# Performance work log

Hardware: AMD Instinct MI355X
Metric: run time of the kernel (lower is better)

Reference implementation:

```python
import math
import jax, jax.numpy as jnp
import numpy as np

B, N, D, H = 8, 512, 1024, 16
HD = D // H
K_DEFAULT, K_MAX, PROX_THR = 8, 12, 20.0


def setup_inputs() -> dict:
    key = jax.random.key(0)
    ks = jax.random.split(key, 12)
    tokens_B = jax.random.normal(ks[0], (B, N, D), dtype=jnp.float32)
    ego_distances = jax.random.uniform(ks[1], (B, N), dtype=jnp.float32)
    ego_mask = jnp.zeros((B, N), dtype=bool).at[:, 0].set(True)  # token 0 is ego
    ego_speed = jax.random.uniform(ks[2], (B,), dtype=jnp.float32)
    s = 1.0 / math.sqrt(D)
    Wq = jax.random.normal(ks[3], (D, D), jnp.float32) * s
    Wk = jax.random.normal(ks[4], (D, D), jnp.float32) * s
    Wv = jax.random.normal(ks[5], (D, D), jnp.float32) * s
    Weq = jax.random.normal(ks[6], (D, D), jnp.float32) * s
    Wo = jax.random.normal(ks[7], (D, D), jnp.float32) * (0.02 * s)
    Dm = D // 4
    W1 = jax.random.normal(ks[8], (Dm, 2), jnp.float32) * (1.0 / math.sqrt(2))
    b1 = jnp.zeros((Dm,), jnp.float32)
    W2 = jax.random.normal(ks[9], (H, Dm), jnp.float32) * (1.0 / math.sqrt(Dm))
    b2 = jnp.zeros((H,), jnp.float32)
    return dict(tokens_B=tokens_B, ego_distances=ego_distances, ego_mask=ego_mask,
                ego_speed=ego_speed, Wq=Wq, Wk=Wk, Wv=Wv, Weq=Weq, Wo=Wo,
                W1=W1, b1=b1, W2=W2, b2=b2)


def _compute_K(ego_speed, ego_distances):
    # deterministic, no-grad lookup (torch: @torch.no_grad)
    n = ego_distances.shape[1]
    close = (ego_distances < PROX_THR).astype(jnp.float32).sum(-1)
    density = close / max(n, 1)
    avg_speed = float(jnp.mean(ego_speed))
    avg_density = float(jnp.mean(density))
    K = K_DEFAULT
    if avg_speed > 15.0:
        K = min(K + 1, K_MAX)
    if avg_density > 0.5:
        K = min(K + 1, K_MAX)
    return min(K, n - 1)


def reference(tokens_B, ego_distances, ego_mask, ego_speed, Wq, Wk, Wv, Weq, Wo, W1, b1, W2, b2):
    b, n, d = tokens_B.shape
    K = _compute_K(ego_speed, ego_distances)
    if K <= 0:
        return jnp.zeros_like(tokens_B)

    # top-K nearest-to-ego neighbors per token, excluding self
    eye = jnp.eye(n, dtype=bool)
    dist_rank = jnp.where(eye[None, :, :], jnp.inf, ego_distances[:, None, :])  # (B,N,N)
    _, topk_idx = jax.lax.top_k(-dist_rank, K)  # (B,N,K) indices of smallest dists

    neighbors = jax.vmap(lambda t, idx: t[idx])(tokens_B, topk_idx)  # (B,N,K,D)

    is_ego = ego_mask.astype(tokens_B.dtype)[..., None]
    Q = (1.0 - is_ego) * (tokens_B @ Wq.T) + is_ego * (tokens_B @ Weq.T)
    Km = neighbors @ Wk.T
    Vm = neighbors @ Wv.T

    Q = Q.reshape(b, n, H, HD).transpose(0, 2, 1, 3)              # (B,H,N,hd)
    Km = Km.reshape(b, n, K, H, HD).transpose(0, 3, 1, 2, 4)      # (B,H,N,K,hd)
    Vm = Vm.reshape(b, n, K, H, HD).transpose(0, 3, 1, 2, 4)

    scores = jnp.einsum('bhnd,bhnkd->bhnk', Q, Km) / math.sqrt(HD)

    # additive pairwise distance bias MLP on (d_i_to_ego, d_j_to_ego)
    d_i = jnp.broadcast_to(ego_distances[:, :, None], (b, n, K))
    d_j = jax.vmap(lambda dd, idx: dd[idx])(ego_distances, topk_idx)
    dist_pair = jnp.stack([d_i, d_j], axis=-1)                    # (B,N,K,2)
    bias = jax.nn.relu(dist_pair @ W1.T + b1) @ W2.T + b2         # (B,N,K,H)
    scores = scores + bias.transpose(0, 3, 1, 2)                  # FIX-1: additive

    attn = jax.nn.softmax(scores, axis=-1)
    out = jnp.einsum('bhnk,bhnkd->bhnd', attn, Vm)
    out = out.transpose(0, 2, 1, 3).reshape(b, n, d)              # FIX-2 axis order
    return out @ Wo.T
```

## Files before the change

kernel.cpp:

```cpp
#include <hip/hip_runtime.h>
#include <math.h>

#define Bn 8
#define Nn 512
#define Dn 1024
#define Hn 16
#define HDn 64
#define KMAX 12
#define NSMAX 13
#define PROX 20.0f

typedef __attribute__((ext_vector_type(8))) short bf16x8;
typedef __attribute__((ext_vector_type(4))) float f32x4;

__device__ __forceinline__ unsigned short f2bf(float f) {
    unsigned int u = __float_as_uint(f);
    return (unsigned short)((u + 0x7FFFu + ((u >> 16) & 1u)) >> 16);
}
__device__ __forceinline__ float bf2f(unsigned short u) {
    return __uint_as_float(((unsigned int)u) << 16);
}

__global__ __launch_bounds__(256) void cvt_meta_kernel(const float* __restrict__ tokens,
                                                       const float* __restrict__ Wq,
                                                       const float* __restrict__ Wo,
                                                       const float* __restrict__ Wk,
                                                       const float* __restrict__ Wv,
                                                       const float* __restrict__ dist,
                                                       const float* __restrict__ speed,
                                                       unsigned short* __restrict__ tok_h,
                                                       unsigned short* __restrict__ wq_h,
                                                       unsigned short* __restrict__ wo_h,
                                                       unsigned short* __restrict__ wkv_h,
                                                       int* __restrict__ meta,
                                                       int* __restrict__ Lidx,
                                                       unsigned short* __restrict__ tok_g) {
    int blk = blockIdx.x;
    if (blk < 8192) {
        const float* src;
        unsigned short* dst;
        int local;
        if (blk < 4096) { src = tokens; dst = tok_h; local = blk; }
        else if (blk < 5120) { src = Wq; dst = wq_h; local = blk - 4096; }
        else if (blk < 6144) { src = Wo; dst = wo_h; local = blk - 5120; }
        else if (blk < 7168) { src = Wk; dst = wkv_h; local = blk - 6144; }
        else { src = Wv; dst = wkv_h + (size_t)Dn * Dn; local = blk - 7168; }
        int i = (local * 256 + threadIdx.x) * 4;
        float4 v = *(const float4*)&src[i];
        ushort4 o;
        o.x = f2bf(v.x); o.y = f2bf(v.y); o.z = f2bf(v.z); o.w = f2bf(v.w);
        *(ushort4*)&dst[i] = o;
        return;
    }
    if (threadIdx.x >= 64) return;
    int lane = threadIdx.x;
    int b = blk - 8192;

    int cnt = 0;
    for (int i = lane; i < Bn * Nn; i += 64) cnt += (dist[i] < PROX) ? 1 : 0;
    for (int off = 32; off; off >>= 1) cnt += __shfl_xor(cnt, off);

    float sp = 0.f;
    for (int i = lane; i < Bn; i += 64) sp += speed[i];
    for (int off = 32; off; off >>= 1) sp += __shfl_xor(sp, off);

    float avg_density = (float)cnt / (float)(Bn * Nn);
    float avg_speed = sp / (float)Bn;
    int K = 8;
    if (avg_speed > 15.0f) K = min(K + 1, KMAX);
    if (avg_density > 0.5f) K = min(K + 1, KMAX);
    K = min(K, Nn - 1);
    if (b == 0 && lane == 0) meta[0] = K;
    int ns = K + 1;

    int sel[NSMAX];
    float dloc[Nn / 64];
    #pragma unroll
    for (int j = 0; j < Nn / 64; ++j) dloc[j] = dist[b * Nn + lane + 64 * j];
    for (int r = 0; r < ns; ++r) {
        float mv = 1e30f;
        int mi = 0;
        #pragma unroll
        for (int j = 0; j < Nn / 64; ++j) {
            if (dloc[j] < mv) { mv = dloc[j]; mi = lane + 64 * j; }
        }
        for (int off = 32; off; off >>= 1) {
            float ov = __shfl_xor(mv, off);
            int oi = __shfl_xor(mi, off);
            if (ov < mv || (ov == mv && oi < mi)) { mv = ov; mi = oi; }
        }
        sel[r] = mi;
        if (lane == 0) Lidx[b * NSMAX + r] = mi;
        if ((mi & 63) == lane) dloc[mi >> 6] = 1e30f;
    }

    const float* srcp = &tokens[(size_t)(b * Nn + sel[0]) * Dn];
    float4 pre[4];
    #pragma unroll
    for (int q = 0; q < 4; ++q) pre[q] = *(const float4*)&srcp[(q * 64 + lane) * 4];
    for (int s = 0; s < ns; ++s) {
        float4 cur[4];
        #pragma unroll
        for (int q = 0; q < 4; ++q) cur[q] = pre[q];
        if (s + 1 < ns) {
            srcp = &tokens[(size_t)(b * Nn + sel[s + 1]) * Dn];
            #pragma unroll
            for (int q = 0; q < 4; ++q) pre[q] = *(const float4*)&srcp[(q * 64 + lane) * 4];
        }
        unsigned short* dst = &tok_g[(size_t)(b * 16 + s) * Dn];
        #pragma unroll
        for (int q = 0; q < 4; ++q) {
            ushort4 o;
            o.x = f2bf(cur[q].x); o.y = f2bf(cur[q].y); o.z = f2bf(cur[q].z); o.w = f2bf(cur[q].w);
            *(ushort4*)&dst[(q * 64 + lane) * 4] = o;
        }
    }
}

__device__ __forceinline__ void gemm_body_s(const unsigned short* A,
                                            const unsigned short* Bm,
                                            float* Cf, unsigned short* Ch,
                                            int Nd, int Kd, int sA, int sB,
                                            int bm, int bn, int mode, int hh,
                                            unsigned short* As, unsigned short* Bs) {
    int t = threadIdx.x;
    int wave = t >> 6, lane = t & 63;
    int wm = wave >> 1, wn = wave & 1;

    int srow = lane >> 2;
    int skoff = (lane & 3) * 8;
    const unsigned short* Ag  = A  + (size_t)(bm + wave * 16 + srow) * sA + skoff;
    const unsigned short* Bg  = Bm + (size_t)(bn + wave * 32 + srow) * sB + skoff;
    const unsigned short* Bg2 = Bg + (size_t)16 * sB;

    f32x4 acc[2][4] = {};
    int fm = lane & 15;
    int fk = (lane >> 4) * 8;

    auto stage = [&](int buf) {
        unsigned short* AsW  = As + buf * 2048 + (wave * 16) * 32;
        unsigned short* BsW  = Bs + buf * 4096 + (wave * 32) * 32;
        __builtin_amdgcn_global_load_lds((const __attribute__((address_space(1))) void*)Ag,
                                         (__attribute__((address_space(3))) void*)AsW, 16, 0, 0);
        __builtin_amdgcn_global_load_lds((const __attribute__((address_space(1))) void*)Bg,
                                         (__attribute__((address_space(3))) void*)BsW, 16, 0, 0);
        __builtin_amdgcn_global_load_lds((const __attribute__((address_space(1))) void*)Bg2,
                                         (__attribute__((address_space(3))) void*)(BsW + 512), 16, 0, 0);
        Ag += 32; Bg += 32; Bg2 += 32;
    };

    int nsteps = Kd >> 5;
    stage(0);
    __syncthreads();
    int cur = 0;
    for (int s = 0; s < nsteps; ++s) {
        if (s + 1 < nsteps) stage(cur ^ 1);
        const unsigned short* Ab = As + cur * 2048;
        const unsigned short* Bb = Bs + cur * 4096;
        bf16x8 af[2], bfr[4];
        #pragma unroll
        for (int mi = 0; mi < 2; ++mi)
            af[mi] = *(const bf16x8*)&Ab[(wm * 32 + mi * 16 + fm) * 32 + fk];
        #pragma unroll
        for (int ni = 0; ni < 4; ++ni)
            bfr[ni] = *(const bf16x8*)&Bb[(wn * 64 + ni * 16 + fm) * 32 + fk];
        #pragma unroll
        for (int mi = 0; mi < 2; ++mi)
            #pragma unroll
            for (int ni = 0; ni < 4; ++ni)
                acc[mi][ni] = __builtin_amdgcn_mfma_f32_16x16x32_bf16(af[mi], bfr[ni], acc[mi][ni], 0, 0, 0);
        __syncthreads();
        cur ^= 1;
    }

    int erow = (lane >> 4) * 4;
    #pragma unroll
    for (int mi = 0; mi < 2; ++mi)
        #pragma unroll
        for (int ni = 0; ni < 4; ++ni)
            #pragma unroll
            for (int r = 0; r < 4; ++r) {
                int row = bm + wm * 32 + mi * 16 + erow + r;
                int col = bn + wn * 64 + ni * 16 + fm;
                if (mode == 0) {
                    Cf[(size_t)row * Nd + col] = acc[mi][ni][r];
                } else if (mode == 1) {
                    Ch[(size_t)row * Nd + col] = f2bf(acc[mi][ni][r]);
                } else {
                    int bb = col >> 4, ss = col & 15;
                    Ch[((size_t)bb * 1024 + row) * 256 + ss * 16 + hh] = f2bf(acc[mi][ni][r]);
                }
            }
}

__global__ __launch_bounds__(256) void proj_fused_kernel(const unsigned short* __restrict__ tok_h,
                                                         const unsigned short* __restrict__ wq_h,
                                                         const unsigned short* __restrict__ tok_g,
                                                         const unsigned short* __restrict__ wkv_h,
                                                         const float* __restrict__ tokens,
                                                         const float* __restrict__ Weq,
                                                         unsigned short* __restrict__ Qbuf_h,
                                                         float* __restrict__ Kproj,
                                                         unsigned short* __restrict__ v_h,
                                                         float* __restrict__ Qego) {
    __shared__ unsigned short As[2 * 64 * 32];
    __shared__ unsigned short Bs[2 * 128 * 32];
    __shared__ float tok[Dn];

    int blk = blockIdx.x;
    if (blk < 16) {
        gemm_body_s(tok_g, wkv_h, Kproj, 0, Dn, Dn, Dn, Dn,
                    (blk >> 3) * 64, (blk & 7) * 128, 0, 0, As, Bs);
    } else if (blk < 32) {
        int idx = blk - 16;
        gemm_body_s(tok_g, wkv_h + (size_t)Dn * Dn, 0, v_h, Dn, Dn, Dn, Dn,
                    (idx >> 3) * 64, (idx & 7) * 128, 1, 0, As, Bs);
    } else if (blk < 544) {
        int idx = blk - 32;
        gemm_body_s(tok_h, wq_h, 0, Qbuf_h, Dn, Dn, Dn, Dn,
                    (idx >> 3) * 64, (idx & 7) * 128, 1, 0, As, Bs);
    } else {
        int blk2 = blk - 544;
        int b = blk2 >> 5, cg = blk2 & 31;
        for (int t = threadIdx.x; t < Dn; t += 256) tok[t] = tokens[(size_t)(b * Nn) * Dn + t];
        __syncthreads();
        int w = threadIdx.x >> 6, lane = threadIdx.x & 63;
        for (int o = 0; o < 8; ++o) {
            int col = cg * 32 + w * 8 + o;
            const float* wr = &Weq[(size_t)col * Dn];
            float sum = 0.f;
            #pragma unroll
            for (int q = 0; q < 4; ++q) {
                float4 w4 = *(const float4*)&wr[q * 256 + lane * 4];
                float4 t4 = *(const float4*)&tok[q * 256 + lane * 4];
                sum += w4.x * t4.x + w4.y * t4.y + w4.z * t4.z + w4.w * t4.w;
            }
            for (int off = 32; off; off >>= 1) sum += __shfl_xor(sum, off);
            if (lane == 0) Qego[(size_t)b * Dn + col] = sum;
        }
    }
}

__global__ __launch_bounds__(256) void vo3_gemm_kernel(const unsigned short* __restrict__ wo_h,
                                                       const unsigned short* __restrict__ v_h,
                                                       unsigned short* __restrict__ Vo3T) {
    __shared__ unsigned short As[2 * 64 * 32];
    __shared__ unsigned short Bs[2 * 128 * 32];
    int h = blockIdx.y;
    gemm_body_s(wo_h + h * HDn, v_h + h * HDn, 0, Vo3T, 0, HDn, Dn, Dn,
                blockIdx.x * 64, 0, 2, h, As, Bs);
}

#define HSTR 264
__global__ __launch_bounds__(64) void attn_kernel(const unsigned short* __restrict__ Qh,
                                                  const float* __restrict__ Qego,
                                                  const float* __restrict__ Kproj,
                                                  const float* __restrict__ dist,
                                                  const float* __restrict__ W1,
                                                  const float* __restrict__ b1,
                                                  const float* __restrict__ W2,
                                                  const float* __restrict__ b2,
                                                  const int* __restrict__ meta,
                                                  const int* __restrict__ Lidx,
                                                  unsigned short* __restrict__ Wt) {
    __shared__ float hid[KMAX * HSTR];
    __shared__ float sc[Hn * NSMAX];
    __shared__ float at[Hn * NSMAX];
    __shared__ int selslot[NSMAX];
    __shared__ int inv[16];
    __shared__ float dj[NSMAX];

    int bi = blockIdx.x;
    int b = bi >> 9;
    int i = bi & (Nn - 1);
    int K = meta[0];
    int ns = K + 1;
    int lane = threadIdx.x;
    int gq = lane >> 4, l = lane & 15;

    float d_i = dist[b * Nn + i];

    {
        int s = lane;
        int jj = (s < ns) ? Lidx[b * NSMAX + s] : -1;
        bool valid = (s < ns) && (jj != i);
        unsigned long long mask = __ballot(valid);
        int rank = __popcll(mask & ((1ull << s) - 1ull));
        bool take = valid && (rank < K);
        if (take) {
            selslot[rank] = s;
            dj[rank] = dist[b * Nn + jj];
        }
        if (s < 16) inv[s] = take ? rank : -1;
    }

    #pragma unroll
    for (int j = 0; j < 4; ++j) {
        int c = lane + 64 * j;
        float2 w01 = *(const float2*)&W1[2 * c];
        float bb = b1[c];
        for (int k = 0; k < K; ++k) {
            float h = w01.x * d_i + w01.y * dj[k] + bb;
            hid[k * HSTR + c] = h > 0.f ? h : 0.f;
        }
    }

    for (int gg = 0; gg < 4; ++gg) {
        int g = gq * 4 + gg;
        float4 qv;
        if (i == 0) {
            qv = *(const float4*)&Qego[(size_t)b * Dn + g * HDn + l * 4];
        } else {
            ushort4 qh = *(const ushort4*)&Qh[(size_t)bi * Dn + g * HDn + l * 4];
            qv.x = bf2f(qh.x); qv.y = bf2f(qh.y); qv.z = bf2f(qh.z); qv.w = bf2f(qh.w);
        }
        float4 w2v[4];
        #pragma unroll
        for (int ii = 0; ii < 4; ++ii)
            w2v[ii] = *(const float4*)&W2[g * 256 + ii * 64 + l * 4];
        float bias0 = b2[g];

        float4 kvn = *(const float4*)&Kproj[(size_t)(b * 16 + selslot[0]) * Dn + g * HDn + l * 4];
        for (int k = 0; k < K; ++k) {
            float4 kv4 = kvn;
            if (k + 1 < K)
                kvn = *(const float4*)&Kproj[(size_t)(b * 16 + selslot[k + 1]) * Dn + g * HDn + l * 4];
            float val = (qv.x * kv4.x + qv.y * kv4.y + qv.z * kv4.z + qv.w * kv4.w) * 0.125f;
            #pragma unroll
            for (int ii = 0; ii < 4; ++ii) {
                float4 h4 = *(const float4*)&hid[k * HSTR + ii * 64 + l * 4];
                val += w2v[ii].x * h4.x + w2v[ii].y * h4.y + w2v[ii].z * h4.z + w2v[ii].w * h4.w;
            }
            val += __shfl_xor(val, 1);
            val += __shfl_xor(val, 2);
            val += __shfl_xor(val, 4);
            val += __shfl_xor(val, 8);
            if (l == 0) sc[g * NSMAX + k] = val + bias0;
        }
    }

    #pragma unroll
    for (int hh = 0; hh < 4; ++hh) {
        int h = gq * 4 + hh;
        int k = l;
        float s = (k < K) ? sc[h * NSMAX + k] : -1e30f;
        float m = s;
        m = fmaxf(m, __shfl_xor(m, 1));
        m = fmaxf(m, __shfl_xor(m, 2));
        m = fmaxf(m, __shfl_xor(m, 4));
        m = fmaxf(m, __shfl_xor(m, 8));
        float e = (k < K) ? __expf(s - m) : 0.f;
        float ssum = e;
        ssum += __shfl_xor(ssum, 1);
        ssum += __shfl_xor(ssum, 2);
        ssum += __shfl_xor(ssum, 4);
        ssum += __shfl_xor(ssum, 8);
        if (k < K) at[h * NSMAX + k] = e / ssum;
    }

    {
        ushort4 o;
        unsigned short* op = (unsigned short*)&o;
        #pragma unroll
        for (int j = 0; j < 4; ++j) {
            int tt = lane * 4 + j;
            int s = tt >> 4, h = tt & 15;
            int k = (s < NSMAX) ? inv[s] : -1;
            float a = (k >= 0) ? at[h * NSMAX + k] : 0.f;
            op[j] = f2bf(a);
        }
        *(ushort4*)&Wt[(size_t)bi * 256 + lane * 4] = o;
    }
}

__global__ __launch_bounds__(256) void final_gemm_kernel(const unsigned short* __restrict__ Wt,
                                                         const unsigned short* __restrict__ Vo3T,
                                                         float* __restrict__ out) {
    __shared__ unsigned short As[2 * 64 * 32];
    __shared__ unsigned short Bs[2 * 128 * 32];
    int rbase = blockIdx.y * 64;
    int b = rbase >> 9;
    int bmloc = rbase & (Nn - 1);
    gemm_body_s(Wt + (size_t)b * Nn * 256,
                Vo3T + (size_t)b * Dn * 256,
                out + (size_t)b * Nn * Dn, 0,
                Dn, 256, 256, 256, bmloc, blockIdx.x * 128, 0, 0, As, Bs);
}

extern "C" void kernel_launch(void* const* d_in, const int* in_sizes, int n_in,
                              void* d_out, int out_size, void* d_ws, size_t ws_size,
                              hipStream_t stream) {
    (void)in_sizes; (void)n_in; (void)out_size; (void)ws_size;
    const float* tokens = (const float*)d_in[0];
    const float* dist   = (const float*)d_in[1];
    const float* speed  = (const float*)d_in[3];
    const float* Wq  = (const float*)d_in[4];
    const float* Wk  = (const float*)d_in[5];
    const float* Wv  = (const float*)d_in[6];
    const float* Weq = (const float*)d_in[7];
    const float* Wo  = (const float*)d_in[8];
    const float* W1  = (const float*)d_in[9];
    const float* b1  = (const float*)d_in[10];
    const float* W2  = (const float*)d_in[11];
    const float* b2  = (const float*)d_in[12];
    float* out = (float*)d_out;

    char* ws = (char*)d_ws;
    const size_t SZ_KP   = (size_t)128 * Dn * sizeof(float);
    const size_t SZ_VH   = (size_t)128 * Dn * sizeof(unsigned short);
    const size_t SZ_V3   = (size_t)Bn * Dn * 256 * sizeof(unsigned short);
    const size_t SZ_WT   = (size_t)Bn * Nn * 256 * sizeof(unsigned short);
    const size_t SZ_QH   = (size_t)Bn * Nn * Dn * sizeof(unsigned short);
    const size_t SZ_BIGH = (size_t)Bn * Nn * Dn * sizeof(unsigned short);
    const size_t SZ_WH   = (size_t)Dn * Dn * sizeof(unsigned short);
    const size_t SZ_TG   = (size_t)128 * Dn * sizeof(unsigned short);
    const size_t SZ_QE   = (size_t)Bn * Dn * sizeof(float);

    size_t off = 0;
    int*   meta  = (int*)(ws + off);  off += 256;
    int*   Lidx  = (int*)(ws + off);  off += 768;
    float* Kproj = (float*)(ws + off); off += SZ_KP;
    float* Qego  = (float*)(ws + off); off += SZ_QE;
    unsigned short* Qbuf_h = (unsigned short*)(ws + off); off += SZ_QH;
    unsigned short* v_h   = (unsigned short*)(ws + off); off += SZ_VH;
    unsigned short* Vo3T  = (unsigned short*)(ws + off); off += SZ_V3;
    unsigned short* Wt    = (unsigned short*)(ws + off); off += SZ_WT;
    unsigned short* tok_h = (unsigned short*)(ws + off); off += SZ_BIGH;
    unsigned short* wq_h  = (unsigned short*)(ws + off); off += SZ_WH;
    unsigned short* wo_h  = (unsigned short*)(ws + off); off += SZ_WH;
    unsigned short* wkv_h = (unsigned short*)(ws + off); off += 2 * SZ_WH;
    unsigned short* tok_g = (unsigned short*)(ws + off); off += SZ_TG;

    cvt_meta_kernel<<<8200, 256, 0, stream>>>(tokens, Wq, Wo, Wk, Wv, dist, speed,
                                              tok_h, wq_h, wo_h, wkv_h, meta, Lidx, tok_g);
    proj_fused_kernel<<<800, 256, 0, stream>>>(tok_h, wq_h, tok_g, wkv_h, tokens, Weq,
                                               Qbuf_h, Kproj, v_h, Qego);
    vo3_gemm_kernel<<<dim3(16, 16), 256, 0, stream>>>(wo_h, v_h, Vo3T);
    attn_kernel<<<Bn * Nn, 64, 0, stream>>>(Qbuf_h, Qego, Kproj, dist, W1, b1, W2, b2,
                                            meta, Lidx, Wt);
    final_gemm_kernel<<<dim3(Dn / 128, (Bn * Nn) / 64), 256, 0, stream>>>(Wt, Vo3T, out);
}
```

Before: 196.3 us.

## Widen attention block to one head per 16 lanes and recompute bias MLP in registers

The attention kernel goes from 64 to 256 threads per token, so each group of 16 lanes handles one head instead of looping over four. The distance-bias MLP hidden layer is no longer staged in a large shared-memory array. Each lane precomputes the d_i part of the first layer in registers and recomputes the ReLU hidden values per neighbor, which removes the roughly 12 KB hid buffer and its LDS traffic. Scores stay in registers, so the sc buffer goes away. The cost is duplicated hidden-layer arithmetic across the 16 heads, plus more registers per thread and two block barriers.

After: 184.2 us. 6.2% less time.

```diff
diff --git a/kernel.cpp b/kernel.cpp
--- a/kernel.cpp
+++ b/kernel.cpp
@@ -251,20 +251,17 @@
                 blockIdx.x * 64, 0, 2, h, As, Bs);
 }
 
-#define HSTR 264
-__global__ __launch_bounds__(64) void attn_kernel(const unsigned short* __restrict__ Qh,
-                                                  const float* __restrict__ Qego,
-                                                  const float* __restrict__ Kproj,
-                                                  const float* __restrict__ dist,
-                                                  const float* __restrict__ W1,
-                                                  const float* __restrict__ b1,
-                                                  const float* __restrict__ W2,
-                                                  const float* __restrict__ b2,
-                                                  const int* __restrict__ meta,
-                                                  const int* __restrict__ Lidx,
-                                                  unsigned short* __restrict__ Wt) {
-    __shared__ float hid[KMAX * HSTR];
-    __shared__ float sc[Hn * NSMAX];
+__global__ __launch_bounds__(256) void attn_kernel(const unsigned short* __restrict__ Qh,
+                                                   const float* __restrict__ Qego,
+                                                   const float* __restrict__ Kproj,
+                                                   const float* __restrict__ dist,
+                                                   const float* __restrict__ W1,
+                                                   const float* __restrict__ b1,
+                                                   const float* __restrict__ W2,
+                                                   const float* __restrict__ b2,
+                                                   const int* __restrict__ meta,
+                                                   const int* __restrict__ Lidx,
+                                                   unsigned short* __restrict__ Wt) {
     __shared__ float at[Hn * NSMAX];
     __shared__ int selslot[NSMAX];
     __shared__ int inv[16];
@@ -275,13 +272,36 @@
     int i = bi & (Nn - 1);
     int K = meta[0];
     int ns = K + 1;
-    int lane = threadIdx.x;
-    int gq = lane >> 4, l = lane & 15;
+    int t = threadIdx.x;
+    int g = t >> 4, l = t & 15;
 
     float d_i = dist[b * Nn + i];
 
-    {
-        int s = lane;
+    float4 qv;
+    if (i == 0) {
+        qv = *(const float4*)&Qego[(size_t)b * Dn + g * HDn + l * 4];
+    } else {
+        ushort4 qh = *(const ushort4*)&Qh[(size_t)bi * Dn + g * HDn + l * 4];
+        qv.x = bf2f(qh.x); qv.y = bf2f(qh.y); qv.z = bf2f(qh.z); qv.w = bf2f(qh.w);
+    }
+    float4 w2v[4];
+    #pragma unroll
+    for (int ii = 0; ii < 4; ++ii)
+        w2v[ii] = *(const float4*)&W2[g * 256 + ii * 64 + l * 4];
+
+    float basec[4][4], w1y[4][4];
+    #pragma unroll
+    for (int ii = 0; ii < 4; ++ii)
+        #pragma unroll
+        for (int j = 0; j < 4; ++j) {
+            int c = ii * 64 + l * 4 + j;
+            float2 w01 = *(const float2*)&W1[2 * c];
+            basec[ii][j] = w01.x * d_i + b1[c];
+            w1y[ii][j] = w01.y;
+        }
+
+    if (t < 64) {
+        int s = t;
         int jj = (s < ns) ? Lidx[b * NSMAX + s] : -1;
         bool valid = (s < ns) && (jj != i);
         unsigned long long mask = __ballot(valid);
@@ -293,83 +313,55 @@
         }
         if (s < 16) inv[s] = take ? rank : -1;
     }
-
-    #pragma unroll
-    for (int j = 0; j < 4; ++j) {
-        int c = lane + 64 * j;
-        float2 w01 = *(const float2*)&W1[2 * c];
-        float bb = b1[c];
-        for (int k = 0; k < K; ++k) {
-            float h = w01.x * d_i + w01.y * dj[k] + bb;
-            hid[k * HSTR + c] = h > 0.f ? h : 0.f;
-        }
-    }
-
-    for (int gg = 0; gg < 4; ++gg) {
-        int g = gq * 4 + gg;
-        float4 qv;
-        if (i == 0) {
-            qv = *(const float4*)&Qego[(size_t)b * Dn + g * HDn + l * 4];
-        } else {
-            ushort4 qh = *(const ushort4*)&Qh[(size_t)bi * Dn + g * HDn + l * 4];
-            qv.x = bf2f(qh.x); qv.y = bf2f(qh.y); qv.z = bf2f(qh.z); qv.w = bf2f(qh.w);
-        }
-        float4 w2v[4];
-        #pragma unroll
-        for (int ii = 0; ii < 4; ++ii)
-            w2v[ii] = *(const float4*)&W2[g * 256 + ii * 64 + l * 4];
+    __syncthreads();
+
+    float myscore = -1e30f;
+    {
         float bias0 = b2[g];
-
         float4 kvn = *(const float4*)&Kproj[(size_t)(b * 16 + selslot[0]) * Dn + g * HDn + l * 4];
         for (int k = 0; k < K; ++k) {
             float4 kv4 = kvn;
             if (k + 1 < K)
                 kvn = *(const float4*)&Kproj[(size_t)(b * 16 + selslot[k + 1]) * Dn + g * HDn + l * 4];
+            float djk = dj[k];
             float val = (qv.x * kv4.x + qv.y * kv4.y + qv.z * kv4.z + qv.w * kv4.w) * 0.125f;
             #pragma unroll
             for (int ii = 0; ii < 4; ++ii) {
-                float4 h4 = *(const float4*)&hid[k * HSTR + ii * 64 + l * 4];
-                val += w2v[ii].x * h4.x + w2v[ii].y * h4.y + w2v[ii].z * h4.z + w2v[ii].w * h4.w;
+                float h0 = basec[ii][0] + w1y[ii][0] * djk; h0 = h0 > 0.f ? h0 : 0.f;
+                float h1 = basec[ii][1] + w1y[ii][1] * djk; h1 = h1 > 0.f ? h1 : 0.f;
+                float h2 = basec[ii][2] + w1y[ii][2] * djk; h2 = h2 > 0.f ? h2 : 0.f;
+                float h3 = basec[ii][3] + w1y[ii][3] * djk; h3 = h3 > 0.f ? h3 : 0.f;
+                val += w2v[ii].x * h0 + w2v[ii].y * h1 + w2v[ii].z * h2 + w2v[ii].w * h3;
             }
             val += __shfl_xor(val, 1);
             val += __shfl_xor(val, 2);
             val += __shfl_xor(val, 4);
             val += __shfl_xor(val, 8);
-            if (l == 0) sc[g * NSMAX + k] = val + bias0;
-        }
-    }
-
-    #pragma unroll
-    for (int hh = 0; hh < 4; ++hh) {
-        int h = gq * 4 + hh;
-        int k = l;
-        float s = (k < K) ? sc[h * NSMAX + k] : -1e30f;
-        float m = s;
+            if (l == k) myscore = val + bias0;
+        }
+    }
+
+    {
+        float m = myscore;
         m = fmaxf(m, __shfl_xor(m, 1));
         m = fmaxf(m, __shfl_xor(m, 2));
         m = fmaxf(m, __shfl_xor(m, 4));
         m = fmaxf(m, __shfl_xor(m, 8));
-        float e = (k < K) ? __expf(s - m) : 0.f;
+        float e = (l < K) ? __expf(myscore - m) : 0.f;
         float ssum = e;
         ssum += __shfl_xor(ssum, 1);
         ssum += __shfl_xor(ssum, 2);
         ssum += __shfl_xor(ssum, 4);
         ssum += __shfl_xor(ssum, 8);
-        if (k < K) at[h * NSMAX + k] = e / ssum;
-    }
+        if (l < K) at[g * NSMAX + l] = e / ssum;
+    }
+    __syncthreads();
 
     {
-        ushort4 o;
-        unsigned short* op = (unsigned short*)&o;
-        #pragma unroll
-        for (int j = 0; j < 4; ++j) {
-            int tt = lane * 4 + j;
-            int s = tt >> 4, h = tt & 15;
-            int k = (s < NSMAX) ? inv[s] : -1;
-            float a = (k >= 0) ? at[h * NSMAX + k] : 0.f;
-            op[j] = f2bf(a);
-        }
-        *(ushort4*)&Wt[(size_t)bi * 256 + lane * 4] = o;
+        int s = t >> 4, h = t & 15;
+        int k = (s < NSMAX) ? inv[s] : -1;
+        float a = (k >= 0) ? at[h * NSMAX + k] : 0.f;
+        Wt[(size_t)bi * 256 + t] = f2bf(a);
     }
 }
 
@@ -436,7 +428,7 @@
     proj_fused_kernel<<<800, 256, 0, stream>>>(tok_h, wq_h, tok_g, wkv_h, tokens, Weq,
                                                Qbuf_h, Kproj, v_h, Qego);
     vo3_gemm_kernel<<<dim3(16, 16), 256, 0, stream>>>(wo_h, v_h, Vo3T);
-    attn_kernel<<<Bn * Nn, 64, 0, stream>>>(Qbuf_h, Qego, Kproj, dist, W1, b1, W2, b2,
-                                            meta, Lidx, Wt);
+    attn_kernel<<<Bn * Nn, 256, 0, stream>>>(Qbuf_h, Qego, Kproj, dist, W1, b1, W2, b2,
+                                             meta, Lidx, Wt);
     final_gemm_kernel<<<dim3(Dn / 128, (Bn * Nn) / 64), 256, 0, stream>>>(Wt, Vo3T, out);
 }
```
